# Kernel tuning notes

Measured on AMD Instinct MI355X. Metric: run time of the kernel, lower is better.

## Reference

```python
import jax, jax.numpy as jnp
import numpy as np

B = 256        # graph pairs
MAX_SET = 64   # nodes per graph == max_set_size (padding is identity)
E = 512        # edges per graph
D = 128        # node_state_dim == av.filters_3
T = 64         # av.transform_dim
N_PROP = 5
N_TIME = 3
TEMP = 0.1
SINK_ITERS = 20
NG = 2 * B
N = NG * MAX_SET
TOT_E = NG * E


def sinkhorn(log_alpha):
    la = log_alpha / TEMP
    for _ in range(SINK_ITERS):
        la = la - jax.nn.logsumexp(la, axis=2, keepdims=True)
        la = la - jax.nn.logsumexp(la, axis=1, keepdims=True)
    return jnp.exp(la)


def setup_inputs() -> dict:
    key = jax.random.key(0)
    ks = jax.random.split(key, 32)

    def lin(k, i, o):
        return jax.random.normal(k, (i, o), jnp.float32) / np.sqrt(i).astype(np.float32)

    node_features = jax.random.normal(ks[0], (N, 32), jnp.float32)
    edge_features = jax.random.normal(ks[1], (TOT_E, 16), jnp.float32)
    offs = jnp.repeat(jnp.arange(NG, dtype=jnp.int32) * MAX_SET, E)
    from_idx = jax.random.randint(ks[2], (TOT_E,), 0, MAX_SET, jnp.int32) + offs
    to_idx = jax.random.randint(ks[3], (TOT_E,), 0, MAX_SET, jnp.int32) + offs
    return {
        "node_features": node_features, "edge_features": edge_features,
        "from_idx": from_idx, "to_idx": to_idx,
        "node_enc_w": lin(ks[4], 32, D), "node_enc_b": jnp.zeros((D,), jnp.float32),
        "edge_enc_w": lin(ks[5], 16, 64), "edge_enc_b": jnp.zeros((64,), jnp.float32),
        "mw1": lin(ks[6], 2 * D + 64, 2 * D), "mb1": jnp.zeros((2 * D,), jnp.float32),
        "mw2": lin(ks[7], 2 * D, D), "mb2": jnp.zeros((D,), jnp.float32),
        "nw1": lin(ks[8], 2 * D, 2 * D), "nb1": jnp.zeros((2 * D,), jnp.float32),
        "nw2": lin(ks[9], 2 * D, D), "nb2": jnp.zeros((D,), jnp.float32),
        "cw1": lin(ks[10], 2 * D, 2 * D), "cb1": jnp.zeros((2 * D,), jnp.float32),
        "cw2": lin(ks[11], 2 * D, D), "cb2": jnp.zeros((D,), jnp.float32),
        "t1w": lin(ks[12], D, T), "t1b": jnp.zeros((T,), jnp.float32),
        "t2w": lin(ks[13], T, T), "t2b": jnp.zeros((T,), jnp.float32),
    }


def reference(node_features, edge_features, from_idx, to_idx,
              node_enc_w, node_enc_b, edge_enc_w, edge_enc_b,
              mw1, mb1, mw2, mb2, nw1, nb1, nw2, nb2,
              cw1, cb1, cw2, cb2, t1w, t1b, t2w, t2b):
    # Encoder (GMN GraphEncoder: linear maps on raw node/edge features)
    h0 = node_features @ node_enc_w + node_enc_b          # [N, D]
    e0 = edge_features @ edge_enc_w + edge_enc_b          # [TOT_E, 64]
    store = jnp.zeros((N, D * (N_PROP + 1)), h0.dtype)    # node_feature_store
    plan = None
    for _t in range(N_TIME):
        h = h0
        parts = [jnp.zeros((N, D), h0.dtype)]             # slot 0 stays zero
        for p in range(1, N_PROP + 1):
            inter = store[:, (p - 1) * D: p * D]          # time_update_idx == 'k_t'
            comb = jax.nn.relu(jnp.concatenate([h, inter], 1) @ cw1 + cb1) @ cw2 + cb2
            # GraphPropLayer: gather -> message MLP -> segment_sum -> node update MLP
            msg_in = jnp.concatenate([comb[from_idx], comb[to_idx], e0], 1)
            messages = jax.nn.relu(msg_in @ mw1 + mb1) @ mw2 + mb2
            agg = jax.ops.segment_sum(messages, to_idx, num_segments=N)
            h = jax.nn.relu(jnp.concatenate([comb, agg], 1) @ nw1 + nb1) @ nw2 + nb2
            parts.append(h)
        store = jnp.concatenate(parts, 1)                 # [N, D*(K+1)]
        # split into padded query/corpus stacks (all graphs have MAX_SET nodes,
        # so F.pad and the size masks are identity here)
        s = store.reshape(NG, MAX_SET, -1)
        q, c = s[0::2], s[1::2]                           # [B, M, D*(K+1)]
        tq = jax.nn.relu(q[:, :, -D:] @ t1w + t1b) @ t2w + t2b
        tc = jax.nn.relu(c[:, :, -D:] @ t1w + t1b) @ t2w + t2b
        sim = jnp.einsum('bqt,bct->bqc', tq, tc)
        plan = sinkhorn(sim)                              # node transport plan [B,M,M]
        qfc = jnp.einsum('bqc,bcd->bqd', plan, c)
        cfq = jnp.einsum('bqc,bqd->bcd', plan, q)
        inter_feats = jnp.stack([qfc, cfq], 1)[:, :, :, D:].reshape(N, N_PROP * D)
        store = store.at[:, D:].set(inter_feats)
    return plan
```

## Files before the change

kernel.cpp:

```cpp
#include <hip/hip_runtime.h>
#include <hip/hip_bf16.h>

#define NNODES   32768
#define NGROUPS  512
#define EPG      512
#define ND       (32768l*128)

__global__ void k_node_enc(const float* __restrict__ nf, const float* __restrict__ w,
                           const float* __restrict__ b, float* __restrict__ h0) {
  int idx = blockIdx.x * 256 + threadIdx.x;
  int row = idx >> 7, col = idx & 127;
  const float* x = nf + row * 32;
  float acc = b[col];
#pragma unroll
  for (int k = 0; k < 32; ++k) acc = fmaf(x[k], w[k * 128 + col], acc);
  h0[idx] = acc;
}

__global__ void k_prep(const float* __restrict__ eew, const float* __restrict__ eeb,
                       const float* __restrict__ mw1, const float* __restrict__ mb1,
                       const float* __restrict__ mb2, const float* __restrict__ nw1,
                       float* __restrict__ Wfold, float* __restrict__ bfold,
                       float* __restrict__ vbias) {
  const int c = threadIdx.x, b = blockIdx.x;
  if (b < 16) {
    float a = 0.f;
    for (int j = 0; j < 64; ++j) a = fmaf(eew[b * 64 + j], mw1[(256 + j) * 256 + c], a);
    Wfold[b * 256 + c] = a;
  } else if (b == 16) {
    float a = mb1[c];
    for (int j = 0; j < 64; ++j) a = fmaf(eeb[j], mw1[(256 + j) * 256 + c], a);
    bfold[c] = a;
  } else {
    float a = 0.f;
    for (int j = 0; j < 128; ++j) a = fmaf(mb2[j], nw1[(128 + j) * 256 + c], a);
    vbias[c] = a;
  }
}

__global__ void k_csr(const int* __restrict__ from_idx, const int* __restrict__ to_idx,
                      const float* __restrict__ ef,
                      int* __restrict__ csr_f, int* __restrict__ rp_g,
                      float* __restrict__ efp, int* __restrict__ deg) {
  __shared__ int cnt[64], rps[65];
  __shared__ int tls[EPG], fls[EPG];
  __shared__ short ord[EPG];
  const int g = blockIdx.x, tid = threadIdx.x;
  const int be = g * EPG, bn = g * 64;
  if (tid < 64) cnt[tid] = 0;
  __syncthreads();
  for (int e = tid; e < EPG; e += 256) {
    int t = to_idx[be + e] - bn;
    tls[e] = t;
    fls[e] = from_idx[be + e] - bn;
    atomicAdd(&cnt[t], 1);
  }
  __syncthreads();
  if (tid == 0) {
    int s = 0;
    for (int i = 0; i < 64; ++i) { rps[i] = s; s += cnt[i]; }
    rps[64] = s;
  }
  __syncthreads();
  if (tid < 64) {
    int pos = rps[tid];
    for (int e = 0; e < EPG; ++e)
      if (tls[e] == tid) ord[pos++] = (short)e;
  }
  __syncthreads();
  for (int ec = tid; ec < EPG; ec += 256) {
    const int eo = ord[ec];
    csr_f[be + ec] = fls[eo];
    const float4* src = (const float4*)&ef[(long)(be + eo) * 16];
    float4* dst = (float4*)&efp[(long)(be + ec) * 16];
    dst[0] = src[0]; dst[1] = src[1]; dst[2] = src[2]; dst[3] = src[3];
  }
  if (tid < 65) rp_g[g * 65 + tid] = rps[tid];
  if (tid < 64) deg[bn + tid] = cnt[tid];
}

template<int K1, bool DEG>
__global__ __launch_bounds__(256, 4)
void k_mlp2g(const float* __restrict__ x0, const float* __restrict__ x1,
             const float* __restrict__ x1b,
             const float* __restrict__ W1a, const float* __restrict__ W1b,
             const float* __restrict__ b1, const int* __restrict__ deg,
             const float* __restrict__ vbias,
             const float* __restrict__ W2, const float* __restrict__ b2,
             float* __restrict__ out) {
  __shared__ __align__(16) float buf[256][36];
  const int tid = threadIdx.x;
  const int row0 = blockIdx.x * 32;

  for (int i = tid; i < 1024; i += 256) {
    const int n = i & 31, q = i >> 5;
    float4 v = *(const float4*)&x0[(long)(row0 + n) * 128 + q * 4];
    buf[q*4+0][n] = v.x; buf[q*4+1][n] = v.y; buf[q*4+2][n] = v.z; buf[q*4+3][n] = v.w;
  }
  if constexpr (K1 == 128) {
    for (int i = tid; i < 1024; i += 256) {
      const int n = i & 31, q = i >> 5;
      float4 v = *(const float4*)&x1[(long)(row0 + n) * 128 + q * 4];
      if (x1b) {
        float4 w = *(const float4*)&x1b[(long)(row0 + n) * 128 + q * 4];
        v.x += w.x; v.y += w.y; v.z += w.z; v.w += w.w;
      }
      buf[128+q*4+0][n] = v.x; buf[128+q*4+1][n] = v.y;
      buf[128+q*4+2][n] = v.z; buf[128+q*4+3][n] = v.w;
    }
  }
  __syncthreads();

  const int tc = tid & 63, rg = tid >> 6;
  const int c0 = tc * 4, r0 = rg * 8;

  float acc[8][4];
  {
    const float4 bv = *(const float4*)&b1[c0];
    if constexpr (DEG) {
      const float4 vb = *(const float4*)&vbias[c0];
#pragma unroll
      for (int r = 0; r < 8; ++r) {
        const float dv = (float)deg[row0 + r0 + r];
        acc[r][0] = fmaf(dv, vb.x, bv.x); acc[r][1] = fmaf(dv, vb.y, bv.y);
        acc[r][2] = fmaf(dv, vb.z, bv.z); acc[r][3] = fmaf(dv, vb.w, bv.w);
      }
    } else {
#pragma unroll
      for (int r = 0; r < 8; ++r) {
        acc[r][0] = bv.x; acc[r][1] = bv.y; acc[r][2] = bv.z; acc[r][3] = bv.w;
      }
    }
  }

#pragma unroll 4
  for (int k = 0; k < 128; ++k) {
    const float4 xa = *(const float4*)&buf[k][r0];
    const float4 xb = *(const float4*)&buf[k][r0 + 4];
    const float4 wv = *(const float4*)&W1a[k * 256 + c0];
    const float xs_[8] = {xa.x, xa.y, xa.z, xa.w, xb.x, xb.y, xb.z, xb.w};
#pragma unroll
    for (int r = 0; r < 8; ++r) {
      acc[r][0] = fmaf(xs_[r], wv.x, acc[r][0]);
      acc[r][1] = fmaf(xs_[r], wv.y, acc[r][1]);
      acc[r][2] = fmaf(xs_[r], wv.z, acc[r][2]);
      acc[r][3] = fmaf(xs_[r], wv.w, acc[r][3]);
    }
  }
  if constexpr (K1 > 0) {
#pragma unroll 4
    for (int k = 0; k < K1; ++k) {
      const float4 xa = *(const float4*)&buf[128 + k][r0];
      const float4 xb = *(const float4*)&buf[128 + k][r0 + 4];
      const float4 wv = *(const float4*)&W1b[k * 256 + c0];
      const float xs_[8] = {xa.x, xa.y, xa.z, xa.w, xb.x, xb.y, xb.z, xb.w};
#pragma unroll
      for (int r = 0; r < 8; ++r) {
        acc[r][0] = fmaf(xs_[r], wv.x, acc[r][0]);
        acc[r][1] = fmaf(xs_[r], wv.y, acc[r][1]);
        acc[r][2] = fmaf(xs_[r], wv.z, acc[r][2]);
        acc[r][3] = fmaf(xs_[r], wv.w, acc[r][3]);
      }
    }
  }
  __syncthreads();
#pragma unroll
  for (int j = 0; j < 4; ++j) {
    float4 lo = make_float4(fmaxf(acc[0][j],0.f), fmaxf(acc[1][j],0.f),
                            fmaxf(acc[2][j],0.f), fmaxf(acc[3][j],0.f));
    float4 hi = make_float4(fmaxf(acc[4][j],0.f), fmaxf(acc[5][j],0.f),
                            fmaxf(acc[6][j],0.f), fmaxf(acc[7][j],0.f));
    *(float4*)&buf[c0 + j][r0]     = lo;
    *(float4*)&buf[c0 + j][r0 + 4] = hi;
  }
  __syncthreads();

  const int c20 = tc * 2;
  float a2[8][2];
#pragma unroll
  for (int r = 0; r < 8; ++r) { a2[r][0] = b2[c20]; a2[r][1] = b2[c20 + 1]; }
#pragma unroll 4
  for (int k = 0; k < 256; ++k) {
    const float4 xa = *(const float4*)&buf[k][r0];
    const float4 xb = *(const float4*)&buf[k][r0 + 4];
    const float2 wv = *(const float2*)&W2[k * 128 + c20];
    const float xs_[8] = {xa.x, xa.y, xa.z, xa.w, xb.x, xb.y, xb.z, xb.w};
#pragma unroll
    for (int r = 0; r < 8; ++r) {
      a2[r][0] = fmaf(xs_[r], wv.x, a2[r][0]);
      a2[r][1] = fmaf(xs_[r], wv.y, a2[r][1]);
    }
  }
#pragma unroll
  for (int r = 0; r < 8; ++r) {
    float2 v = make_float2(a2[r][0], a2[r][1]);
    *(float2*)&out[(long)(row0 + r0 + r) * 128 + c20] = v;
  }
}

__global__ __launch_bounds__(256, 3)
void k_edge(const float* __restrict__ comb, const float* __restrict__ efp,
            const float* __restrict__ mw1, const float* __restrict__ mw2,
            const float* __restrict__ Wfold, const float* __restrict__ bfold,
            const int* __restrict__ csr_f, const int* __restrict__ rp_g,
            float* __restrict__ aggM) {
  __shared__ __align__(16) float cA[64 * 64];
  __shared__ __align__(16) float U[128 * 64];
  __shared__ int fl[EPG];
  __shared__ int rp[65];
  float* ct = U;
  float* ag = U;

  const int tid = threadIdx.x;
  const int g = blockIdx.x, half = blockIdx.y;
  const int be = g * EPG, bn = g * 64;

  for (int i = tid; i < EPG; i += 256) fl[i] = csr_f[be + i];
  if (tid < 65) rp[tid] = rp_g[g * 65 + tid];

  const int ng = tid >> 4, cg = tid & 15;
  const int n0 = ng * 4, cq = cg * 4;

  float aM[4][8];
#pragma unroll
  for (int i = 0; i < 4; ++i)
#pragma unroll
    for (int j = 0; j < 8; ++j) aM[i][j] = 0.f;

  for (int cbi = 0; cbi < 2; ++cbi) {
    const int col0 = (half * 2 + cbi) * 64;
    __syncthreads();
    for (int i = tid; i < 2048; i += 256) {
      const int n = i & 63, q = i >> 6;
      float4 v = *(const float4*)&comb[(long)(bn + n) * 128 + q * 4];
      ct[(q*4+0)*64 + n] = v.x; ct[(q*4+1)*64 + n] = v.y;
      ct[(q*4+2)*64 + n] = v.z; ct[(q*4+3)*64 + n] = v.w;
    }
    __syncthreads();
    float accA[4][4], accB[4][4];
#pragma unroll
    for (int i = 0; i < 4; ++i)
#pragma unroll
      for (int j = 0; j < 4; ++j) { accA[i][j] = 0.f; accB[i][j] = 0.f; }
    {
      const int c0 = col0 + cq;
#pragma unroll 2
      for (int k = 0; k < 128; ++k) {
        const float4 xv = *(const float4*)&ct[k * 64 + n0];
        const float4 wa = *(const float4*)&mw1[k * 256 + c0];
        const float4 wb = *(const float4*)&mw1[(128 + k) * 256 + c0];
        const float xs_[4] = {xv.x, xv.y, xv.z, xv.w};
#pragma unroll
        for (int i = 0; i < 4; ++i) {
          accA[i][0] = fmaf(xs_[i], wa.x, accA[i][0]);
          accA[i][1] = fmaf(xs_[i], wa.y, accA[i][1]);
          accA[i][2] = fmaf(xs_[i], wa.z, accA[i][2]);
          accA[i][3] = fmaf(xs_[i], wa.w, accA[i][3]);
          accB[i][0] = fmaf(xs_[i], wb.x, accB[i][0]);
          accB[i][1] = fmaf(xs_[i], wb.y, accB[i][1]);
          accB[i][2] = fmaf(xs_[i], wb.z, accB[i][2]);
          accB[i][3] = fmaf(xs_[i], wb.w, accB[i][3]);
        }
      }
    }
    __syncthreads();
#pragma unroll
    for (int i = 0; i < 4; ++i)
      *(float4*)&cA[(n0 + i) * 64 + cq] =
        make_float4(accA[i][0], accA[i][1], accA[i][2], accA[i][3]);
    float4 Wf[16];
#pragma unroll
    for (int k = 0; k < 16; ++k) Wf[k] = *(const float4*)&Wfold[k * 256 + col0 + cq];
    const float4 bf = *(const float4*)&bfold[col0 + cq];
    __syncthreads();

#pragma unroll
    for (int i = 0; i < 4; ++i) {
      const int n = n0 + i;
      float4 acc = make_float4(0.f, 0.f, 0.f, 0.f);
      const float4 cB = make_float4(accB[i][0], accB[i][1], accB[i][2], accB[i][3]);
      const int e1 = rp[n + 1];
      for (int e = rp[n]; e < e1; ++e) {
        const int f = fl[e];
        const float* er = efp + (long)(be + e) * 16;
        float4 h = bf;
#pragma unroll
        for (int kq = 0; kq < 4; ++kq) {
          const float4 e4 = *(const float4*)(er + kq * 4);
          const float ev[4] = {e4.x, e4.y, e4.z, e4.w};
#pragma unroll
          for (int s = 0; s < 4; ++s) {
            const float4 w = Wf[kq * 4 + s];
            h.x = fmaf(ev[s], w.x, h.x); h.y = fmaf(ev[s], w.y, h.y);
            h.z = fmaf(ev[s], w.z, h.z); h.w = fmaf(ev[s], w.w, h.w);
          }
        }
        const float4 va = *(const float4*)&cA[f * 64 + cq];
        acc.x += fmaxf(h.x + va.x + cB.x, 0.f);
        acc.y += fmaxf(h.y + va.y + cB.y, 0.f);
        acc.z += fmaxf(h.z + va.z + cB.z, 0.f);
        acc.w += fmaxf(h.w + va.w + cB.w, 0.f);
      }
      *(float4*)&ag[n * 64 + cq] = acc;
    }
    __syncthreads();

    {
      const int c2 = cg * 8;
#pragma unroll 2
      for (int kk = 0; kk < 64; ++kk) {
        const float4 w0 = *(const float4*)&mw2[(col0 + kk) * 128 + c2];
        const float4 w1 = *(const float4*)&mw2[(col0 + kk) * 128 + c2 + 4];
#pragma unroll
        for (int i = 0; i < 4; ++i) {
          const float x = ag[(n0 + i) * 64 + kk];
          aM[i][0] = fmaf(x, w0.x, aM[i][0]); aM[i][1] = fmaf(x, w0.y, aM[i][1]);
          aM[i][2] = fmaf(x, w0.z, aM[i][2]); aM[i][3] = fmaf(x, w0.w, aM[i][3]);
          aM[i][4] = fmaf(x, w1.x, aM[i][4]); aM[i][5] = fmaf(x, w1.y, aM[i][5]);
          aM[i][6] = fmaf(x, w1.z, aM[i][6]); aM[i][7] = fmaf(x, w1.w, aM[i][7]);
        }
      }
    }
  }
  float* aggMh = aggM + (long)half * ND;
#pragma unroll
  for (int i = 0; i < 4; ++i) {
    *(float4*)&aggMh[(long)(bn + n0 + i) * 128 + cg * 8]     = *(float4*)&aM[i][0];
    *(float4*)&aggMh[(long)(bn + n0 + i) * 128 + cg * 8 + 4] = *(float4*)&aM[i][4];
  }
}

__global__ void k_tfeat(const float* __restrict__ x,
                        const float* __restrict__ t1w, const float* __restrict__ t1b,
                        const float* __restrict__ t2w, const float* __restrict__ t2b,
                        float* __restrict__ tf) {
  __shared__ float xs[4][128];
  __shared__ float ys[4][64];
  const int tid = threadIdx.x;
  const long row0 = (long)blockIdx.x * 4;
  for (int i = tid; i < 512; i += 256)
    xs[i >> 7][i & 127] = x[(row0 + (i >> 7)) * 128 + (i & 127)];
  __syncthreads();
  const int r = tid >> 6, c = tid & 63;
  float acc = t1b[c];
#pragma unroll 4
  for (int k = 0; k < 128; ++k) acc = fmaf(xs[r][k], t1w[k * 64 + c], acc);
  ys[r][c] = fmaxf(acc, 0.f);
  __syncthreads();
  float a2 = t2b[c];
#pragma unroll 4
  for (int k = 0; k < 64; ++k) a2 = fmaf(ys[r][k], t2w[k * 64 + c], a2);
  tf[(row0 + r) * 64 + c] = a2;
}

__global__ void k_sim(const float* __restrict__ tf, float* __restrict__ sim) {
  const int b = blockIdx.x, tid = threadIdx.x;
  __shared__ float tq[64][65];
  __shared__ float tcs[64][65];
  for (int i = tid; i < 4096; i += 256) {
    tq[i >> 6][i & 63]  = tf[(long)b * 8192 + i];
    tcs[i >> 6][i & 63] = tf[(long)b * 8192 + 4096 + i];
  }
  __syncthreads();
  const int m = tid >> 2, j0 = (tid & 3) * 16;
#pragma unroll
  for (int j = 0; j < 16; ++j) {
    float a = 0.f;
#pragma unroll 4
    for (int k = 0; k < 64; ++k) a = fmaf(tq[m][k], tcs[j0 + j][k], a);
    sim[(long)b * 4096 + m * 64 + j0 + j] = a;
  }
}

__global__ void k_sink(float* __restrict__ sim, float* __restrict__ outp) {
  const int b = blockIdx.x, tid = threadIdx.x;
  __shared__ float la[64][65];
  const float C = 14.426950408889634f;
  for (int i = tid; i < 4096; i += 256)
    la[i >> 6][i & 63] = sim[(long)b * 4096 + i] * C;
  __syncthreads();
  const int r4 = tid >> 2, l4 = tid & 3;
  for (int it = 0; it < 20; ++it) {
    {
      float m = -3.4e38f;
#pragma unroll
      for (int i = 0; i < 16; ++i) m = fmaxf(m, la[r4][l4 + 4 * i]);
      m = fmaxf(m, __shfl_xor(m, 1)); m = fmaxf(m, __shfl_xor(m, 2));
      float s = 0.f;
#pragma unroll
      for (int i = 0; i < 16; ++i) s += exp2f(la[r4][l4 + 4 * i] - m);
      s += __shfl_xor(s, 1); s += __shfl_xor(s, 2);
      const float lse = m + log2f(s);
#pragma unroll
      for (int i = 0; i < 16; ++i) la[r4][l4 + 4 * i] -= lse;
    }
    __syncthreads();
    {
      float m = -3.4e38f;
#pragma unroll
      for (int i = 0; i < 16; ++i) m = fmaxf(m, la[l4 + 4 * i][r4]);
      m = fmaxf(m, __shfl_xor(m, 1)); m = fmaxf(m, __shfl_xor(m, 2));
      float s = 0.f;
#pragma unroll
      for (int i = 0; i < 16; ++i) s += exp2f(la[l4 + 4 * i][r4] - m);
      s += __shfl_xor(s, 1); s += __shfl_xor(s, 2);
      const float lse = m + log2f(s);
#pragma unroll
      for (int i = 0; i < 16; ++i) la[l4 + 4 * i][r4] -= lse;
    }
    __syncthreads();
  }
  for (int i = tid; i < 4096; i += 256) {
    const float v = exp2f(la[i >> 6][i & 63]);
    outp[(long)b * 4096 + i] = v;
    sim[(long)b * 4096 + i] = v;
  }
}

__global__ void k_mix(const float* __restrict__ plan, const float* __restrict__ src,
                      float* __restrict__ dst) {
  const int b = blockIdx.x, tid = threadIdx.x;
  __shared__ float pl[64][65];
  __shared__ float qs[64][128];
  __shared__ float cs[64][128];
  const long qbase = (long)(2 * b) * 64, cbase = qbase + 64;
  for (int i = tid; i < 4096; i += 256) pl[i >> 6][i & 63] = plan[(long)b * 4096 + i];
  for (int i = tid; i < 8192; i += 256) {
    qs[i >> 7][i & 127] = src[qbase * 128 + i];
    cs[i >> 7][i & 127] = src[cbase * 128 + i];
  }
  __syncthreads();
  const int d = tid & 127, m0 = (tid >> 7) * 32;
  for (int m = m0; m < m0 + 32; ++m) {
    float a = 0.f;
#pragma unroll 4
    for (int j = 0; j < 64; ++j) a = fmaf(pl[m][j], cs[j][d], a);
    dst[(qbase + m) * 128 + d] = a;
  }
  for (int j = m0; j < m0 + 32; ++j) {
    float a = 0.f;
#pragma unroll 4
    for (int m = 0; m < 64; ++m) a = fmaf(pl[m][j], qs[m][d], a);
    dst[(cbase + j) * 128 + d] = a;
  }
}

extern "C" void kernel_launch(void* const* d_in, const int* in_sizes, int n_in,
                              void* d_out, int out_size, void* d_ws, size_t ws_size,
                              hipStream_t stream) {
  const float* nf  = (const float*)d_in[0];
  const float* ef  = (const float*)d_in[1];
  const int* from_idx = (const int*)d_in[2];
  const int* to_idx   = (const int*)d_in[3];
  const float* new_w = (const float*)d_in[4];
  const float* new_b = (const float*)d_in[5];
  const float* eew = (const float*)d_in[6];
  const float* eeb = (const float*)d_in[7];
  const float* mw1 = (const float*)d_in[8];
  const float* mb1 = (const float*)d_in[9];
  const float* mw2 = (const float*)d_in[10];
  const float* mb2 = (const float*)d_in[11];
  const float* nw1 = (const float*)d_in[12];
  const float* nb1 = (const float*)d_in[13];
  const float* nw2 = (const float*)d_in[14];
  const float* nb2 = (const float*)d_in[15];
  const float* cw1 = (const float*)d_in[16];
  const float* cb1 = (const float*)d_in[17];
  const float* cw2 = (const float*)d_in[18];
  const float* cb2 = (const float*)d_in[19];
  const float* t1w = (const float*)d_in[20];
  const float* t1b = (const float*)d_in[21];
  const float* t2w = (const float*)d_in[22];
  const float* t2b = (const float*)d_in[23];

  float* W = (float*)d_ws;
  float* h0     = W;
  float* comb   = h0 + ND;
  float* aggM0  = comb + ND;
  float* aggM1  = aggM0 + ND;
  float* parts  = aggM1 + ND;
  float* efp    = parts + 5 * ND;
  float* Wfold  = efp + 262144l * 16;
  float* bfold  = Wfold + 4096;
  float* vbias  = bfold + 256;
  int*   deg    = (int*)(vbias + 256);
  int*   csr_f  = deg + 32768;
  int*   rp_g   = csr_f + 262144;
  float* tf     = aggM0;
  float* sim    = aggM0 + 2097152;
  float* outp   = (float*)d_out;

  k_prep<<<18, 256, 0, stream>>>(eew, eeb, mw1, mb1, mb2, nw1, Wfold, bfold, vbias);
  k_csr<<<512, 256, 0, stream>>>(from_idx, to_idx, ef, csr_f, rp_g, efp, deg);
  k_node_enc<<<16384, 256, 0, stream>>>(nf, new_w, new_b, h0);

  for (int t = 0; t < 3; ++t) {
    const float* hprev = h0;
    for (int p = 1; p <= 5; ++p) {
      if (t > 0 && p > 1)
        k_mlp2g<128, false><<<1024, 256, 0, stream>>>(hprev, parts + (long)(p - 1) * ND,
                                                      nullptr, cw1, cw1 + 128 * 256,
                                                      cb1, nullptr, nullptr, cw2, cb2, comb);
      else
        k_mlp2g<0, false><<<1024, 256, 0, stream>>>(hprev, nullptr, nullptr, cw1, nullptr,
                                                    cb1, nullptr, nullptr, cw2, cb2, comb);
      k_edge<<<dim3(512, 2), 256, 0, stream>>>(comb, efp, mw1, mw2, Wfold, bfold,
                                               csr_f, rp_g, aggM0);
      float* hnew = parts + (long)(p - 1) * ND;
      k_mlp2g<128, true><<<1024, 256, 0, stream>>>(comb, aggM0, aggM1,
                                                   nw1, nw1 + 128 * 256,
                                                   nb1, deg, vbias, nw2, nb2, hnew);
      hprev = hnew;
    }
    k_tfeat<<<8192, 256, 0, stream>>>(parts + 4 * ND, t1w, t1b, t2w, t2b, tf);
    k_sim<<<256, 256, 0, stream>>>(tf, sim);
    k_sink<<<256, 256, 0, stream>>>(sim, outp);
    if (t < 2) {
      for (int pi = 3; pi >= 0; --pi)
        k_mix<<<256, 256, 0, stream>>>(sim, parts + (long)pi * ND, parts + (long)(pi + 1) * ND);
    }
  }
}
```

Baseline: 6.776 ms.

## Run node MLPs on bf16 MFMA with three-way split emulating fp32

Replaces the scalar-FMA two-layer MLP kernel with an MFMA version. Activations and weights are split into high/mid/low bf16 parts, and six bf16 MFMA products per tile approximate fp32 accuracy. Weights are pre-split and transposed once per call by a new kernel. This moves the dense MLP arithmetic from the vector ALUs onto the matrix cores. The cost is extra LDS for the three split planes (occupancy bound lowered to 2) and conversion work.

```diff
diff --git a/kernel.cpp b/kernel.cpp
--- a/kernel.cpp
+++ b/kernel.cpp
@@ -5,6 +5,23 @@
 #define NGROUPS  512
 #define EPG      512
 #define ND       (32768l*128)
+
+typedef __attribute__((ext_vector_type(4))) float f32x4;
+typedef __attribute__((ext_vector_type(8))) short bf16x8;
+
+__device__ __forceinline__ short f2bf(float x) {
+  unsigned u = __float_as_uint(x);
+  unsigned r = (u + 0x7FFF + ((u >> 16) & 1)) >> 16;
+  return (short)r;
+}
+__device__ __forceinline__ float bf2f(short h) {
+  return __uint_as_float(((unsigned)(unsigned short)h) << 16);
+}
+__device__ __forceinline__ void split3(float x, short* ph, short* pm, short* pl, int idx) {
+  short h = f2bf(x); float r1 = x - bf2f(h);
+  short m = f2bf(r1); float r2 = r1 - bf2f(m);
+  ph[idx] = h; pm[idx] = m; pl[idx] = f2bf(r2);
+}
 
 __global__ void k_node_enc(const float* __restrict__ nf, const float* __restrict__ w,
                            const float* __restrict__ b, float* __restrict__ h0) {
@@ -38,6 +55,16 @@
   }
 }
 
+__global__ void k_wsplit3(const float* __restrict__ W, int C, int Kd,
+                          short* __restrict__ th, short* __restrict__ tm,
+                          short* __restrict__ tl) {
+  const int c = blockIdx.x;
+  for (int k = threadIdx.x; k < Kd; k += 256) {
+    float w = W[(long)k * C + c];
+    split3(w, th, tm, tl, c * 256 + k);
+  }
+}
+
 __global__ void k_csr(const int* __restrict__ from_idx, const int* __restrict__ to_idx,
                       const float* __restrict__ ef,
                       int* __restrict__ csr_f, int* __restrict__ rp_g,
@@ -79,123 +106,159 @@
   if (tid < 64) deg[bn + tid] = cnt[tid];
 }
 
-template<int K1, bool DEG>
-__global__ __launch_bounds__(256, 4)
-void k_mlp2g(const float* __restrict__ x0, const float* __restrict__ x1,
+template<int KTOT, bool DEG, bool SUM2>
+__global__ __launch_bounds__(256, 2)
+void k_mlp2m(const float* __restrict__ x0, const float* __restrict__ x1,
              const float* __restrict__ x1b,
-             const float* __restrict__ W1a, const float* __restrict__ W1b,
+             const short* __restrict__ W1h, const short* __restrict__ W1m,
+             const short* __restrict__ W1l,
              const float* __restrict__ b1, const int* __restrict__ deg,
              const float* __restrict__ vbias,
-             const float* __restrict__ W2, const float* __restrict__ b2,
-             float* __restrict__ out) {
-  __shared__ __align__(16) float buf[256][36];
+             const short* __restrict__ W2h, const short* __restrict__ W2m,
+             const short* __restrict__ W2l,
+             const float* __restrict__ b2, float* __restrict__ out) {
+  __shared__ short xh[32 * 264];
+  __shared__ short xm[32 * 264];
+  __shared__ short xl[32 * 264];
+  __shared__ int degs[32];
   const int tid = threadIdx.x;
-  const int row0 = blockIdx.x * 32;
-
-  for (int i = tid; i < 1024; i += 256) {
-    const int n = i & 31, q = i >> 5;
-    float4 v = *(const float4*)&x0[(long)(row0 + n) * 128 + q * 4];
-    buf[q*4+0][n] = v.x; buf[q*4+1][n] = v.y; buf[q*4+2][n] = v.z; buf[q*4+3][n] = v.w;
-  }
-  if constexpr (K1 == 128) {
-    for (int i = tid; i < 1024; i += 256) {
-      const int n = i & 31, q = i >> 5;
-      float4 v = *(const float4*)&x1[(long)(row0 + n) * 128 + q * 4];
-      if (x1b) {
-        float4 w = *(const float4*)&x1b[(long)(row0 + n) * 128 + q * 4];
+  const long row0 = (long)blockIdx.x * 32;
+
+  for (int i = tid; i < 32 * 32; i += 256) {
+    const int r = i >> 5, q = i & 31;
+    float4 v = *(const float4*)&x0[(row0 + r) * 128 + q * 4];
+    const int base = r * 264 + q * 4;
+    split3(v.x, xh, xm, xl, base + 0);
+    split3(v.y, xh, xm, xl, base + 1);
+    split3(v.z, xh, xm, xl, base + 2);
+    split3(v.w, xh, xm, xl, base + 3);
+  }
+  if constexpr (KTOT == 256) {
+    for (int i = tid; i < 32 * 32; i += 256) {
+      const int r = i >> 5, q = i & 31;
+      float4 v = *(const float4*)&x1[(row0 + r) * 128 + q * 4];
+      if constexpr (SUM2) {
+        float4 w = *(const float4*)&x1b[(row0 + r) * 128 + q * 4];
         v.x += w.x; v.y += w.y; v.z += w.z; v.w += w.w;
       }
-      buf[128+q*4+0][n] = v.x; buf[128+q*4+1][n] = v.y;
-      buf[128+q*4+2][n] = v.z; buf[128+q*4+3][n] = v.w;
-    }
-  }
-  __syncthreads();
-
-  const int tc = tid & 63, rg = tid >> 6;
-  const int c0 = tc * 4, r0 = rg * 8;
-
-  float acc[8][4];
-  {
-    const float4 bv = *(const float4*)&b1[c0];
+      const int base = r * 264 + 128 + q * 4;
+      split3(v.x, xh, xm, xl, base + 0);
+      split3(v.y, xh, xm, xl, base + 1);
+      split3(v.z, xh, xm, xl, base + 2);
+      split3(v.w, xh, xm, xl, base + 3);
+    }
+  }
+  if constexpr (DEG) { if (tid < 32) degs[tid] = deg[row0 + tid]; }
+  __syncthreads();
+
+  const int lane = tid & 63, wid = tid >> 6;
+  const int lr = lane & 15;
+  const int lk = (lane >> 4) * 8;
+  const int rsub = (lane >> 4) * 4;
+
+  f32x4 acc[2][4];
+#pragma unroll
+  for (int fc = 0; fc < 4; ++fc) {
+    const int col = wid * 64 + fc * 16 + lr;
+    const float bv = b1[col];
+#pragma unroll
+    for (int fr = 0; fr < 2; ++fr) acc[fr][fc] = {bv, bv, bv, bv};
     if constexpr (DEG) {
-      const float4 vb = *(const float4*)&vbias[c0];
-#pragma unroll
-      for (int r = 0; r < 8; ++r) {
-        const float dv = (float)deg[row0 + r0 + r];
-        acc[r][0] = fmaf(dv, vb.x, bv.x); acc[r][1] = fmaf(dv, vb.y, bv.y);
-        acc[r][2] = fmaf(dv, vb.z, bv.z); acc[r][3] = fmaf(dv, vb.w, bv.w);
+      const float vb = vbias[col];
+#pragma unroll
+      for (int fr = 0; fr < 2; ++fr)
+#pragma unroll
+        for (int r = 0; r < 4; ++r)
+          acc[fr][fc][r] += (float)degs[fr * 16 + rsub + r] * vb;
+    }
+  }
+
+  for (int ks = 0; ks < KTOT / 32; ++ks) {
+    const int k0 = ks * 32 + lk;
+    bf16x8 ah[2], am[2], al[2];
+#pragma unroll
+    for (int fr = 0; fr < 2; ++fr) {
+      const int ab = (fr * 16 + lr) * 264 + k0;
+      ah[fr] = *(const bf16x8*)&xh[ab];
+      am[fr] = *(const bf16x8*)&xm[ab];
+      al[fr] = *(const bf16x8*)&xl[ab];
+    }
+#pragma unroll
+    for (int fc = 0; fc < 4; ++fc) {
+      const long wrow = (long)(wid * 64 + fc * 16 + lr) * 256 + k0;
+      const bf16x8 bh = *(const bf16x8*)&W1h[wrow];
+      const bf16x8 bm = *(const bf16x8*)&W1m[wrow];
+      const bf16x8 bl = *(const bf16x8*)&W1l[wrow];
+#pragma unroll
+      for (int fr = 0; fr < 2; ++fr) {
+        acc[fr][fc] = __builtin_amdgcn_mfma_f32_16x16x32_bf16(ah[fr], bh, acc[fr][fc], 0, 0, 0);
+        acc[fr][fc] = __builtin_amdgcn_mfma_f32_16x16x32_bf16(ah[fr], bm, acc[fr][fc], 0, 0, 0);
+        acc[fr][fc] = __builtin_amdgcn_mfma_f32_16x16x32_bf16(am[fr], bh, acc[fr][fc], 0, 0, 0);
+        acc[fr][fc] = __builtin_amdgcn_mfma_f32_16x16x32_bf16(ah[fr], bl, acc[fr][fc], 0, 0, 0);
+        acc[fr][fc] = __builtin_amdgcn_mfma_f32_16x16x32_bf16(am[fr], bm, acc[fr][fc], 0, 0, 0);
+        acc[fr][fc] = __builtin_amdgcn_mfma_f32_16x16x32_bf16(al[fr], bh, acc[fr][fc], 0, 0, 0);
       }
-    } else {
-#pragma unroll
-      for (int r = 0; r < 8; ++r) {
-        acc[r][0] = bv.x; acc[r][1] = bv.y; acc[r][2] = bv.z; acc[r][3] = bv.w;
+    }
+  }
+  __syncthreads();
+
+#pragma unroll
+  for (int fr = 0; fr < 2; ++fr)
+#pragma unroll
+    for (int fc = 0; fc < 4; ++fc) {
+      const int col = wid * 64 + fc * 16 + lr;
+#pragma unroll
+      for (int r = 0; r < 4; ++r) {
+        const int row = fr * 16 + rsub + r;
+        float v = fmaxf(acc[fr][fc][r], 0.f);
+        split3(v, xh, xm, xl, row * 264 + col);
       }
     }
-  }
-
-#pragma unroll 4
-  for (int k = 0; k < 128; ++k) {
-    const float4 xa = *(const float4*)&buf[k][r0];
-    const float4 xb = *(const float4*)&buf[k][r0 + 4];
-    const float4 wv = *(const float4*)&W1a[k * 256 + c0];
-    const float xs_[8] = {xa.x, xa.y, xa.z, xa.w, xb.x, xb.y, xb.z, xb.w};
-#pragma unroll
-    for (int r = 0; r < 8; ++r) {
-      acc[r][0] = fmaf(xs_[r], wv.x, acc[r][0]);
-      acc[r][1] = fmaf(xs_[r], wv.y, acc[r][1]);
-      acc[r][2] = fmaf(xs_[r], wv.z, acc[r][2]);
-      acc[r][3] = fmaf(xs_[r], wv.w, acc[r][3]);
-    }
-  }
-  if constexpr (K1 > 0) {
-#pragma unroll 4
-    for (int k = 0; k < K1; ++k) {
-      const float4 xa = *(const float4*)&buf[128 + k][r0];
-      const float4 xb = *(const float4*)&buf[128 + k][r0 + 4];
-      const float4 wv = *(const float4*)&W1b[k * 256 + c0];
-      const float xs_[8] = {xa.x, xa.y, xa.z, xa.w, xb.x, xb.y, xb.z, xb.w};
-#pragma unroll
-      for (int r = 0; r < 8; ++r) {
-        acc[r][0] = fmaf(xs_[r], wv.x, acc[r][0]);
-        acc[r][1] = fmaf(xs_[r], wv.y, acc[r][1]);
-        acc[r][2] = fmaf(xs_[r], wv.z, acc[r][2]);
-        acc[r][3] = fmaf(xs_[r], wv.w, acc[r][3]);
+  __syncthreads();
+
+  f32x4 acc2[2][2];
+#pragma unroll
+  for (int fc = 0; fc < 2; ++fc) {
+    const float bv = b2[wid * 32 + fc * 16 + lr];
+#pragma unroll
+    for (int fr = 0; fr < 2; ++fr) acc2[fr][fc] = {bv, bv, bv, bv};
+  }
+  for (int ks = 0; ks < 8; ++ks) {
+    const int k0 = ks * 32 + lk;
+    bf16x8 ah[2], am[2], al[2];
+#pragma unroll
+    for (int fr = 0; fr < 2; ++fr) {
+      const int ab = (fr * 16 + lr) * 264 + k0;
+      ah[fr] = *(const bf16x8*)&xh[ab];
+      am[fr] = *(const bf16x8*)&xm[ab];
+      al[fr] = *(const bf16x8*)&xl[ab];
+    }
+#pragma unroll
+    for (int fc = 0; fc < 2; ++fc) {
+      const long wrow = (long)(wid * 32 + fc * 16 + lr) * 256 + k0;
+      const bf16x8 bh = *(const bf16x8*)&W2h[wrow];
+      const bf16x8 bm = *(const bf16x8*)&W2m[wrow];
+      const bf16x8 bl = *(const bf16x8*)&W2l[wrow];
+#pragma unroll
+      for (int fr = 0; fr < 2; ++fr) {
+        acc2[fr][fc] = __builtin_amdgcn_mfma_f32_16x16x32_bf16(ah[fr], bh, acc2[fr][fc], 0, 0, 0);
+        acc2[fr][fc] = __builtin_amdgcn_mfma_f32_16x16x32_bf16(ah[fr], bm, acc2[fr][fc], 0, 0, 0);
+        acc2[fr][fc] = __builtin_amdgcn_mfma_f32_16x16x32_bf16(am[fr], bh, acc2[fr][fc], 0, 0, 0);
+        acc2[fr][fc] = __builtin_amdgcn_mfma_f32_16x16x32_bf16(ah[fr], bl, acc2[fr][fc], 0, 0, 0);
+        acc2[fr][fc] = __builtin_amdgcn_mfma_f32_16x16x32_bf16(am[fr], bm, acc2[fr][fc], 0, 0, 0);
+        acc2[fr][fc] = __builtin_amdgcn_mfma_f32_16x16x32_bf16(al[fr], bh, acc2[fr][fc], 0, 0, 0);
       }
     }
   }
-  __syncthreads();
-#pragma unroll
-  for (int j = 0; j < 4; ++j) {
-    float4 lo = make_float4(fmaxf(acc[0][j],0.f), fmaxf(acc[1][j],0.f),
-                            fmaxf(acc[2][j],0.f), fmaxf(acc[3][j],0.f));
-    float4 hi = make_float4(fmaxf(acc[4][j],0.f), fmaxf(acc[5][j],0.f),
-                            fmaxf(acc[6][j],0.f), fmaxf(acc[7][j],0.f));
-    *(float4*)&buf[c0 + j][r0]     = lo;
-    *(float4*)&buf[c0 + j][r0 + 4] = hi;
-  }
-  __syncthreads();
-
-  const int c20 = tc * 2;
-  float a2[8][2];
-#pragma unroll
-  for (int r = 0; r < 8; ++r) { a2[r][0] = b2[c20]; a2[r][1] = b2[c20 + 1]; }
-#pragma unroll 4
-  for (int k = 0; k < 256; ++k) {
-    const float4 xa = *(const float4*)&buf[k][r0];
-    const float4 xb = *(const float4*)&buf[k][r0 + 4];
-    const float2 wv = *(const float2*)&W2[k * 128 + c20];
-    const float xs_[8] = {xa.x, xa.y, xa.z, xa.w, xb.x, xb.y, xb.z, xb.w};
-#pragma unroll
-    for (int r = 0; r < 8; ++r) {
-      a2[r][0] = fmaf(xs_[r], wv.x, a2[r][0]);
-      a2[r][1] = fmaf(xs_[r], wv.y, a2[r][1]);
-    }
-  }
-#pragma unroll
-  for (int r = 0; r < 8; ++r) {
-    float2 v = make_float2(a2[r][0], a2[r][1]);
-    *(float2*)&out[(long)(row0 + r0 + r) * 128 + c20] = v;
-  }
+#pragma unroll
+  for (int fr = 0; fr < 2; ++fr)
+#pragma unroll
+    for (int fc = 0; fc < 2; ++fc) {
+      const int col = wid * 32 + fc * 16 + lr;
+#pragma unroll
+      for (int r = 0; r < 4; ++r)
+        out[(row0 + fr * 16 + rsub + r) * 128 + col] = acc2[fr][fc][r];
+    }
 }
 
 __global__ __launch_bounds__(256, 3)
@@ -486,30 +549,50 @@
   int*   deg    = (int*)(vbias + 256);
   int*   csr_f  = deg + 32768;
   int*   rp_g   = csr_f + 262144;
+  short* cw1t_h = (short*)(rp_g + 33280);
+  short* cw1t_m = cw1t_h + 65536;
+  short* cw1t_l = cw1t_m + 65536;
+  short* nw1t_h = cw1t_l + 65536;
+  short* nw1t_m = nw1t_h + 65536;
+  short* nw1t_l = nw1t_m + 65536;
+  short* cw2t_h = nw1t_l + 65536;
+  short* cw2t_m = cw2t_h + 32768;
+  short* cw2t_l = cw2t_m + 32768;
+  short* nw2t_h = cw2t_l + 32768;
+  short* nw2t_m = nw2t_h + 32768;
+  short* nw2t_l = nw2t_m + 32768;
   float* tf     = aggM0;
   float* sim    = aggM0 + 2097152;
   float* outp   = (float*)d_out;
 
   k_prep<<<18, 256, 0, stream>>>(eew, eeb, mw1, mb1, mb2, nw1, Wfold, bfold, vbias);
   k_csr<<<512, 256, 0, stream>>>(from_idx, to_idx, ef, csr_f, rp_g, efp, deg);
+  k_wsplit3<<<256, 256, 0, stream>>>(cw1, 256, 256, cw1t_h, cw1t_m, cw1t_l);
+  k_wsplit3<<<256, 256, 0, stream>>>(nw1, 256, 256, nw1t_h, nw1t_m, nw1t_l);
+  k_wsplit3<<<128, 256, 0, stream>>>(cw2, 128, 256, cw2t_h, cw2t_m, cw2t_l);
+  k_wsplit3<<<128, 256, 0, stream>>>(nw2, 128, 256, nw2t_h, nw2t_m, nw2t_l);
   k_node_enc<<<16384, 256, 0, stream>>>(nf, new_w, new_b, h0);
 
   for (int t = 0; t < 3; ++t) {
     const float* hprev = h0;
     for (int p = 1; p <= 5; ++p) {
       if (t > 0 && p > 1)
-        k_mlp2g<128, false><<<1024, 256, 0, stream>>>(hprev, parts + (long)(p - 1) * ND,
-                                                      nullptr, cw1, cw1 + 128 * 256,
-                                                      cb1, nullptr, nullptr, cw2, cb2, comb);
+        k_mlp2m<256, false, false><<<1024, 256, 0, stream>>>(
+            hprev, parts + (long)(p - 1) * ND, nullptr,
+            cw1t_h, cw1t_m, cw1t_l, cb1, nullptr, nullptr,
+            cw2t_h, cw2t_m, cw2t_l, cb2, comb);
       else
-        k_mlp2g<0, false><<<1024, 256, 0, stream>>>(hprev, nullptr, nullptr, cw1, nullptr,
-                                                    cb1, nullptr, nullptr, cw2, cb2, comb);
+        k_mlp2m<128, false, false><<<1024, 256, 0, stream>>>(
+            hprev, nullptr, nullptr,
+            cw1t_h, cw1t_m, cw1t_l, cb1, nullptr, nullptr,
+            cw2t_h, cw2t_m, cw2t_l, cb2, comb);
       k_edge<<<dim3(512, 2), 256, 0, stream>>>(comb, efp, mw1, mw2, Wfold, bfold,
                                                csr_f, rp_g, aggM0);
       float* hnew = parts + (long)(p - 1) * ND;
-      k_mlp2g<128, true><<<1024, 256, 0, stream>>>(comb, aggM0, aggM1,
-                                                   nw1, nw1 + 128 * 256,
-                                                   nb1, deg, vbias, nw2, nb2, hnew);
+      k_mlp2m<256, true, true><<<1024, 256, 0, stream>>>(
+          comb, aggM0, aggM1,
+          nw1t_h, nw1t_m, nw1t_l, nb1, deg, vbias,
+          nw2t_h, nw2t_m, nw2t_l, nb2, hnew);
       hprev = hnew;
     }
     k_tfeat<<<8192, 256, 0, stream>>>(parts + 4 * ND, t1w, t1b, t2w, t2b, tf);
```

New measurement: 6.685 ms. About the same (-1.3%).
